# Optimization experiments

Hardware: AMD Instinct MI355X
Metric: run time of the kernel (lower is better)

Reference implementation:

```python
import jax, jax.numpy as jnp
import numpy as np
from jax import lax

B, Q, N, C = 64, 900, 100, 256
EPS = 1e-6
BOX_W, GIOU_W, CLS_W = 5.0, 2.0, 1.0


def cxcywh_to_xyxy(b):
    cx, cy, w, h = jnp.split(b, 4, axis=-1)
    return jnp.concatenate([cx - 0.5 * w, cy - 0.5 * h, cx + 0.5 * w, cy + 0.5 * h], axis=-1)


def xyxy_to_cxcywh(b):
    x0, y0, x1, y1 = jnp.split(b, 4, axis=-1)
    return jnp.concatenate([(x0 + x1) / 2, (y0 + y1) / 2, x1 - x0, y1 - y0], axis=-1)


def pairwise_giou(b1, b2):
    # b1: [Q,4] xyxy, b2: [N,4] xyxy -> [Q,N]
    area1 = (b1[:, 2] - b1[:, 0]) * (b1[:, 3] - b1[:, 1])
    area2 = (b2[:, 2] - b2[:, 0]) * (b2[:, 3] - b2[:, 1])
    lt = jnp.maximum(b1[:, None, :2], b2[None, :, :2])
    rb = jnp.minimum(b1[:, None, 2:], b2[None, :, 2:])
    wh = jnp.clip(rb - lt, 0.0)
    inter = wh[..., 0] * wh[..., 1]
    union = area1[:, None] + area2[None, :] - inter
    iou = inter / (union + EPS)
    lt2 = jnp.minimum(b1[:, None, :2], b2[None, :, :2])
    rb2 = jnp.maximum(b1[:, None, 2:], b2[None, :, 2:])
    wh2 = jnp.clip(rb2 - lt2, 0.0)
    area = wh2[..., 0] * wh2[..., 1]
    return iou - (area - union) / (area + EPS)


def elementwise_giou(b1, b2):
    # b1, b2: [..., 4] xyxy -> [...]; equals diag of pairwise giou
    area1 = (b1[..., 2] - b1[..., 0]) * (b1[..., 3] - b1[..., 1])
    area2 = (b2[..., 2] - b2[..., 0]) * (b2[..., 3] - b2[..., 1])
    lt = jnp.maximum(b1[..., :2], b2[..., :2])
    rb = jnp.minimum(b1[..., 2:], b2[..., 2:])
    wh = jnp.clip(rb - lt, 0.0)
    inter = wh[..., 0] * wh[..., 1]
    union = area1 + area2 - inter
    iou = inter / (union + EPS)
    lt2 = jnp.minimum(b1[..., :2], b2[..., :2])
    rb2 = jnp.maximum(b1[..., 2:], b2[..., 2:])
    wh2 = jnp.clip(rb2 - lt2, 0.0)
    area = wh2[..., 0] * wh2[..., 1]
    return iou - (area - union) / (area + EPS)


def greedy_match(iou_img):
    # iou_img: [Q, N]; sequentially assign best unused pred to each target (in target order)
    def step(used, col):
        idx = jnp.argmax(jnp.where(used, -jnp.inf, col))
        return used.at[idx].set(True), idx
    used0 = jnp.zeros(iou_img.shape[0], dtype=bool)
    _, idxs = lax.scan(step, used0, iou_img.T)
    return idxs  # [N]


def setup_inputs() -> dict:
    key = jax.random.key(0)
    k1, k2, k3, k4, k5 = jax.random.split(key, 5)
    pb = jax.random.uniform(k1, (B, Q, 4), dtype=jnp.float32)
    # cxcywh with small positive w,h
    pred_boxes = jnp.concatenate([pb[..., :2], pb[..., 2:] * 0.3 + 0.01], axis=-1)
    pred_logits = jax.random.normal(k2, (B, Q, C), dtype=jnp.float32)
    lo = jax.random.uniform(k3, (B, N, 2), dtype=jnp.float32) * 0.8
    sz = jax.random.uniform(k4, (B, N, 2), dtype=jnp.float32) * 0.2 + 0.01
    target_boxes = jnp.concatenate([lo, lo + sz], axis=-1)  # valid xyxy in [0,1]
    target_labels = jax.random.randint(k5, (B, N), 0, C)
    return {"pred_boxes": pred_boxes, "pred_logits": pred_logits,
            "target_boxes": target_boxes, "target_labels": target_labels}


def reference(pred_boxes, pred_logits, target_boxes, target_labels):
    pred_xyxy = cxcywh_to_xyxy(pred_boxes)                      # [B,Q,4]
    iou = lax.stop_gradient(jax.vmap(pairwise_giou)(pred_xyxy, target_boxes))  # [B,Q,N]
    idxs = jax.vmap(greedy_match)(iou)                          # [B,N] matched pred indices

    mpb = jnp.take_along_axis(pred_boxes, idxs[..., None], axis=1)   # [B,N,4] cxcywh
    mtb = xyxy_to_cxcywh(target_boxes)                               # [B,N,4]
    l1_loss = jnp.abs(mpb - mtb).sum()

    giou = elementwise_giou(cxcywh_to_xyxy(mpb), target_boxes)       # [B,N]
    giou_loss = (1.0 - giou).sum()

    ml = jnp.take_along_axis(pred_logits, idxs[..., None], axis=1)   # [B,N,C]
    tdist = jax.nn.one_hot(target_labels, ml.shape[-1], dtype=ml.dtype)
    # stable BCE-with-logits, reduction='sum'
    cls_loss = (jnp.maximum(ml, 0.0) - ml * tdist + jnp.log1p(jnp.exp(-jnp.abs(ml)))).sum()

    num_boxes = idxs.shape[0] * idxs.shape[1]
    return (BOX_W * l1_loss + GIOU_W * giou_loss + CLS_W * cls_loss) / num_boxes
```

## Files before the change

kernel.cpp:

```cpp
#include <hip/hip_runtime.h>
#include <math.h>

constexpr int B_ = 64, Q_ = 900, N_ = 100, C_ = 256;
constexpr float EPSF = 1e-6f;
constexpr float BOX_W = 5.0f, GIOU_W = 2.0f, CLS_W = 1.0f;
constexpr int KP = 15;
constexpr int K_ = 8;
typedef unsigned long long u64;
typedef unsigned int u32;

__device__ __forceinline__ float giou_f(float px0, float py0, float px1, float py1, float pa,
                                        float tx0, float ty0, float tx1, float ty1, float ta) {
    float ltx = fmaxf(px0, tx0), lty = fmaxf(py0, ty0);
    float rbx = fminf(px1, tx1), rby = fminf(py1, ty1);
    float w = fmaxf(rbx - ltx, 0.0f), h = fmaxf(rby - lty, 0.0f);
    float inter = w * h;
    float uni = pa + ta - inter;
    float iou = inter / (uni + EPSF);
    float ex0 = fminf(px0, tx0), ey0 = fminf(py0, ty0);
    float ex1 = fmaxf(px1, tx1), ey1 = fmaxf(py1, ty1);
    float ew = fmaxf(ex1 - ex0, 0.0f), eh = fmaxf(ey1 - ey0, 0.0f);
    float earea = ew * eh;
    return iou - (earea - uni) / (earea + EPSF);
}

__device__ __forceinline__ u32 f2ord(float f) {
    u32 u = __float_as_uint(f);
    return (u & 0x80000000u) ? ~u : (u | 0x80000000u);
}
__device__ __forceinline__ u64 mkkey(float g, int q) {
    return ((u64)f2ord(g) << 32) | (u32)(~(u32)q);
}
__device__ __forceinline__ int keyidx(u64 k) { return (int)(~(u32)k); }
__device__ __forceinline__ u64 umax64(u64 a, u64 b) { return a > b ? a : b; }
__device__ __forceinline__ u64 umin64(u64 a, u64 b) { return a > b ? b : a; }

__global__ __launch_bounds__(256) void cand_kernel(
    const float* __restrict__ pred_boxes,
    const float* __restrict__ target_boxes,
    u32* __restrict__ cands)
{
    const int blk = blockIdx.x;
    const int b = blk / 25;
    const int wave = threadIdx.x >> 6;
    const int lane = threadIdx.x & 63;
    const int n = (blk % 25) * 4 + wave;
    const int bn = b * N_ + n;

    const float* t = target_boxes + (size_t)bn * 4;
    float tx0 = t[0], ty0 = t[1], tx1 = t[2], ty1 = t[3];
    float ta = (tx1 - tx0) * (ty1 - ty0);

    const float4* pbv = (const float4*)(pred_boxes + (size_t)b * Q_ * 4);
    u64 a0 = 0, a1 = 0, a2 = 0, a3 = 0, a4 = 0, a5 = 0, a6 = 0, a7 = 0;
    #pragma unroll
    for (int k = 0; k < KP; ++k) {
        int q = lane + (k << 6);
        if (q < Q_) {
            float4 c = pbv[q];
            float x0 = c.x - 0.5f * c.z, y0 = c.y - 0.5f * c.w;
            float x1 = c.x + 0.5f * c.z, y1 = c.y + 0.5f * c.w;
            float pa = (x1 - x0) * (y1 - y0);
            float g = giou_f(x0, y0, x1, y1, pa, tx0, ty0, tx1, ty1, ta);
            u64 kk = mkkey(g, q);
            a7 = umax64(a7, umin64(a6, kk));
            a6 = umax64(a6, umin64(a5, kk));
            a5 = umax64(a5, umin64(a4, kk));
            a4 = umax64(a4, umin64(a3, kk));
            a3 = umax64(a3, umin64(a2, kk));
            a2 = umax64(a2, umin64(a1, kk));
            a1 = umax64(a1, umin64(a0, kk));
            a0 = umax64(a0, kk);
        }
    }
    u32* outp = cands + (size_t)bn * K_;
    #pragma unroll
    for (int j = 0; j < K_; ++j) {
        u64 m = a0;
        #pragma unroll
        for (int off = 32; off >= 1; off >>= 1) {
            u64 o = __shfl_xor(m, off);
            if (o > m) m = o;
        }
        if (lane == 0) outp[j] = (u32)keyidx(m);
        if (a0 == m) {
            a0 = a1; a1 = a2; a2 = a3; a3 = a4; a4 = a5; a5 = a6; a6 = a7; a7 = 0;
        }
    }
}

__global__ __launch_bounds__(64, 1) void match_kernel(
    const float* __restrict__ pred_boxes,
    const float* __restrict__ target_boxes,
    const u32*   __restrict__ cands,
    int* __restrict__ matches,
    double* __restrict__ box_part)
{
    const int b = blockIdx.x;
    const int lane = threadIdx.x;

    __shared__ float tx0s[N_], ty0s[N_], tx1s[N_], ty1s[N_], tas[N_];
    __shared__ int   s_ms[N_];
    __shared__ u32   s_used[32];
    __shared__ u32   s_claim[1024];

    for (int i = lane; i < 1024; i += 64) s_claim[i] = 0u;
    if (lane < 32) s_used[lane] = 0u;
    for (int n = lane; n < N_; n += 64) {
        const float* t = target_boxes + (size_t)(b * N_ + n) * 4;
        float x0 = t[0], y0 = t[1], x1 = t[2], y1 = t[3];
        tx0s[n] = x0; ty0s[n] = y0; tx1s[n] = x1; ty1s[n] = y1;
        tas[n] = (x1 - x0) * (y1 - y0);
    }

    int cA[K_], cB[K_];
    {
        const u32* p = cands + (size_t)(b * N_ + lane) * K_;
        #pragma unroll
        for (int j = 0; j < K_; ++j) cA[j] = (int)p[j];
    }
    #pragma unroll
    for (int j = 0; j < K_; ++j) cB[j] = 0;
    if (lane + 64 < N_) {
        const u32* p = cands + (size_t)(b * N_ + lane + 64) * K_;
        #pragma unroll
        for (int j = 0; j < K_; ++j) cB[j] = (int)p[j];
    }

    const float4* pbv = (const float4*)(pred_boxes + (size_t)b * Q_ * 4);
    bool activeA = true;
    bool activeB = (lane + 64 < N_);
    __syncthreads();

    int round = 1;
    while (__ballot(activeA) | __ballot(activeB)) {
        int pickA = -1, pickB = -1;
        #pragma unroll
        for (int j = 0; j < K_; ++j) {
            int ia = cA[j];
            bool availA = !((s_used[ia >> 5] >> (ia & 31)) & 1u);
            if (pickA < 0 && availA) pickA = ia;
            int ib = cB[j];
            bool availB = !((s_used[ib >> 5] >> (ib & 31)) & 1u);
            if (pickB < 0 && availB) pickB = ib;
        }
        u64 fm = __ballot(activeA && pickA < 0);
        while (fm) {
            int c = (int)__builtin_ctzll(fm);
            float tx0 = tx0s[c], ty0 = ty0s[c], tx1 = tx1s[c], ty1 = ty1s[c], ta = tas[c];
            u64 bk = 0ull;
            #pragma unroll
            for (int k = 0; k < KP; ++k) {
                int q = lane + (k << 6);
                if (q < Q_ && !((s_used[q >> 5] >> (q & 31)) & 1u)) {
                    float4 cc = pbv[q];
                    float x0 = cc.x - 0.5f * cc.z, y0 = cc.y - 0.5f * cc.w;
                    float x1 = cc.x + 0.5f * cc.z, y1 = cc.y + 0.5f * cc.w;
                    float pa = (x1 - x0) * (y1 - y0);
                    float g = giou_f(x0, y0, x1, y1, pa, tx0, ty0, tx1, ty1, ta);
                    u64 kk = mkkey(g, q);
                    if (kk > bk) bk = kk;
                }
            }
            #pragma unroll
            for (int off = 32; off >= 1; off >>= 1) {
                u64 o = __shfl_xor(bk, off);
                if (o > bk) bk = o;
            }
            if (lane == c) pickA = keyidx(bk);
            fm &= fm - 1;
        }
        fm = __ballot(activeB && pickB < 0);
        while (fm) {
            int c = (int)__builtin_ctzll(fm);
            int n = c + 64;
            float tx0 = tx0s[n], ty0 = ty0s[n], tx1 = tx1s[n], ty1 = ty1s[n], ta = tas[n];
            u64 bk = 0ull;
            #pragma unroll
            for (int k = 0; k < KP; ++k) {
                int q = lane + (k << 6);
                if (q < Q_ && !((s_used[q >> 5] >> (q & 31)) & 1u)) {
                    float4 cc = pbv[q];
                    float x0 = cc.x - 0.5f * cc.z, y0 = cc.y - 0.5f * cc.w;
                    float x1 = cc.x + 0.5f * cc.z, y1 = cc.y + 0.5f * cc.w;
                    float pa = (x1 - x0) * (y1 - y0);
                    float g = giou_f(x0, y0, x1, y1, pa, tx0, ty0, tx1, ty1, ta);
                    u64 kk = mkkey(g, q);
                    if (kk > bk) bk = kk;
                }
            }
            #pragma unroll
            for (int off = 32; off >= 1; off >>= 1) {
                u64 o = __shfl_xor(bk, off);
                if (o > bk) bk = o;
            }
            if (lane == c) pickB = keyidx(bk);
            fm &= fm - 1;
        }
        u32 tagA = ((u32)round << 16) | (0xFFFFu - (u32)lane);
        u32 tagB = ((u32)round << 16) | (0xFFFFu - (u32)(lane + 64));
        if (activeA) atomicMax(&s_claim[pickA], tagA);
        if (activeB) atomicMax(&s_claim[pickB], tagB);
        __syncthreads();
        if (activeA && s_claim[pickA] == tagA) {
            s_ms[lane] = pickA;
            atomicOr(&s_used[pickA >> 5], 1u << (pickA & 31));
            activeA = false;
        }
        if (activeB && s_claim[pickB] == tagB) {
            s_ms[lane + 64] = pickB;
            atomicOr(&s_used[pickB >> 5], 1u << (pickB & 31));
            activeB = false;
        }
        __syncthreads();
        ++round;
    }

    double acc = 0.0;
    for (int n = lane; n < N_; n += 64) {
        int q = s_ms[n];
        matches[b * N_ + n] = q;
        float4 c = pbv[q];
        float tx0 = tx0s[n], ty0 = ty0s[n], tx1 = tx1s[n], ty1 = ty1s[n];
        float tcx = (tx0 + tx1) * 0.5f, tcy = (ty0 + ty1) * 0.5f;
        float tw = tx1 - tx0, th = ty1 - ty0;
        float l1 = fabsf(c.x - tcx) + fabsf(c.y - tcy) + fabsf(c.z - tw) + fabsf(c.w - th);
        float x0 = c.x - 0.5f * c.z, y0 = c.y - 0.5f * c.w;
        float x1 = c.x + 0.5f * c.z, y1 = c.y + 0.5f * c.w;
        float pa2 = (x1 - x0) * (y1 - y0);
        float g = giou_f(x0, y0, x1, y1, pa2, tx0, ty0, tx1, ty1, tas[n]);
        acc += (double)(BOX_W * l1) + (double)(GIOU_W * (1.0f - g));
    }
    #pragma unroll
    for (int off = 32; off >= 1; off >>= 1) acc += __shfl_xor(acc, off);
    if (lane == 0) box_part[b] = acc;
}

__global__ __launch_bounds__(64) void bce_kernel(
    const float* __restrict__ pred_logits,
    const int* __restrict__ target_labels,
    const int* __restrict__ matches,
    double* __restrict__ part)
{
    const int bn = blockIdx.x;
    const int b = bn / N_;
    const int lane = threadIdx.x;
    const int q = matches[bn];
    const int lab = target_labels[bn];

    const float4* row = (const float4*)(pred_logits + ((size_t)(b * Q_ + q)) * C_);
    float4 v = row[lane];
    int base = lane * 4;
    float xs[4] = {v.x, v.y, v.z, v.w};
    double acc = 0.0;
    #pragma unroll
    for (int j = 0; j < 4; ++j) {
        float x = xs[j];
        float t = (base + j == lab) ? 1.0f : 0.0f;
        float term = fmaxf(x, 0.0f) - x * t + log1pf(expf(-fabsf(x)));
        acc += (double)term;
    }
    #pragma unroll
    for (int off = 32; off >= 1; off >>= 1) acc += __shfl_xor(acc, off);
    if (lane == 0) part[bn] = acc * (double)CLS_W;
}

__global__ __launch_bounds__(256) void finalize_kernel(
    const double* __restrict__ bce_part,
    const double* __restrict__ box_part,
    float* __restrict__ out)
{
    const int tid = threadIdx.x;
    double acc = 0.0;
    for (int i = tid; i < B_ * N_; i += 256) acc += bce_part[i];
    if (tid < B_) acc += box_part[tid];
    __shared__ double red[256];
    red[tid] = acc;
    __syncthreads();
    #pragma unroll
    for (int s = 128; s >= 1; s >>= 1) {
        if (tid < s) red[tid] += red[tid + s];
        __syncthreads();
    }
    if (tid == 0) out[0] = (float)(red[0] / (double)(B_ * N_));
}

extern "C" void kernel_launch(void* const* d_in, const int* in_sizes, int n_in,
                              void* d_out, int out_size, void* d_ws, size_t ws_size,
                              hipStream_t stream) {
    const float* pred_boxes    = (const float*)d_in[0];
    const float* pred_logits   = (const float*)d_in[1];
    const float* target_boxes  = (const float*)d_in[2];
    const int*   target_labels = (const int*)d_in[3];
    float* out = (float*)d_out;

    char* ws = (char*)d_ws;
    u32*    cands    = (u32*)(ws);
    int*    matches  = (int*)(ws + 204800);
    double* bce_part = (double*)(ws + 230400);
    double* box_part = (double*)(ws + 281600);

    hipLaunchKernelGGL(cand_kernel, dim3(1600), dim3(256), 0, stream,
                       pred_boxes, target_boxes, cands);
    hipLaunchKernelGGL(match_kernel, dim3(B_), dim3(64), 0, stream,
                       pred_boxes, target_boxes, cands, matches, box_part);
    hipLaunchKernelGGL(bce_kernel, dim3(B_ * N_), dim3(64), 0, stream,
                       pred_logits, target_labels, matches, bce_part);
    hipLaunchKernelGGL(finalize_kernel, dim3(1), dim3(256), 0, stream,
                       bce_part, box_part, out);
}
```

Baseline: 46.01 us.

## Fuse matching, BCE and final reduction into one kernel with last-block finalize

```diff
diff --git a/kernel.cpp b/kernel.cpp
--- a/kernel.cpp
+++ b/kernel.cpp
@@ -32,14 +32,15 @@
     return ((u64)f2ord(g) << 32) | (u32)(~(u32)q);
 }
 __device__ __forceinline__ int keyidx(u64 k) { return (int)(~(u32)k); }
-__device__ __forceinline__ u64 umax64(u64 a, u64 b) { return a > b ? a : b; }
-__device__ __forceinline__ u64 umin64(u64 a, u64 b) { return a > b ? b : a; }
 
 __global__ __launch_bounds__(256) void cand_kernel(
     const float* __restrict__ pred_boxes,
     const float* __restrict__ target_boxes,
-    u32* __restrict__ cands)
+    u32* __restrict__ cands,
+    u32* __restrict__ cnt)
 {
+    if (blockIdx.x == 0 && threadIdx.x == 0) *cnt = 0u;
+
     const int blk = blockIdx.x;
     const int b = blk / 25;
     const int wave = threadIdx.x >> 6;
@@ -52,65 +53,81 @@
     float ta = (tx1 - tx0) * (ty1 - ty0);
 
     const float4* pbv = (const float4*)(pred_boxes + (size_t)b * Q_ * 4);
-    u64 a0 = 0, a1 = 0, a2 = 0, a3 = 0, a4 = 0, a5 = 0, a6 = 0, a7 = 0;
+
+    u32 ordv[KP];
     #pragma unroll
     for (int k = 0; k < KP; ++k) {
         int q = lane + (k << 6);
+        ordv[k] = 0u;
         if (q < Q_) {
             float4 c = pbv[q];
             float x0 = c.x - 0.5f * c.z, y0 = c.y - 0.5f * c.w;
             float x1 = c.x + 0.5f * c.z, y1 = c.y + 0.5f * c.w;
             float pa = (x1 - x0) * (y1 - y0);
             float g = giou_f(x0, y0, x1, y1, pa, tx0, ty0, tx1, ty1, ta);
-            u64 kk = mkkey(g, q);
-            a7 = umax64(a7, umin64(a6, kk));
-            a6 = umax64(a6, umin64(a5, kk));
-            a5 = umax64(a5, umin64(a4, kk));
-            a4 = umax64(a4, umin64(a3, kk));
-            a3 = umax64(a3, umin64(a2, kk));
-            a2 = umax64(a2, umin64(a1, kk));
-            a1 = umax64(a1, umin64(a0, kk));
-            a0 = umax64(a0, kk);
-        }
-    }
-    u32* outp = cands + (size_t)bn * K_;
+            ordv[k] = f2ord(g);
+        }
+    }
+
+    u32 alive = 0x7FFFu;
+    u32 o8[K_];
     #pragma unroll
     for (int j = 0; j < K_; ++j) {
-        u64 m = a0;
+        u32 bo = 0u; int bk = 0;
+        #pragma unroll
+        for (int k = 0; k < KP; ++k) {
+            bool tk = (((alive >> k) & 1u) != 0u) && (ordv[k] > bo);
+            bo = tk ? ordv[k] : bo;
+            bk = tk ? k : bk;
+        }
+        u64 myk = ((u64)bo << 32) | (u32)(~(u32)(lane + (bk << 6)));
+        u64 m = myk;
         #pragma unroll
         for (int off = 32; off >= 1; off >>= 1) {
             u64 o = __shfl_xor(m, off);
             if (o > m) m = o;
         }
-        if (lane == 0) outp[j] = (u32)keyidx(m);
-        if (a0 == m) {
-            a0 = a1; a1 = a2; a2 = a3; a3 = a4; a4 = a5; a5 = a6; a6 = a7; a7 = 0;
-        }
-    }
-}
-
-__global__ __launch_bounds__(64, 1) void match_kernel(
+        if (myk == m) alive &= ~(1u << bk);
+        o8[j] = (u32)(~(u32)m);
+    }
+    if (lane == 0) {
+        uint4* outp = (uint4*)(cands + (size_t)bn * K_);
+        outp[0] = make_uint4(o8[0], o8[1], o8[2], o8[3]);
+        outp[1] = make_uint4(o8[4], o8[5], o8[6], o8[7]);
+    }
+}
+
+__global__ __launch_bounds__(256) void fused_kernel(
     const float* __restrict__ pred_boxes,
+    const float* __restrict__ pred_logits,
     const float* __restrict__ target_boxes,
+    const int*   __restrict__ target_labels,
     const u32*   __restrict__ cands,
-    int* __restrict__ matches,
-    double* __restrict__ box_part)
+    double* __restrict__ partial,
+    u32* __restrict__ cnt,
+    float* __restrict__ out)
 {
     const int b = blockIdx.x;
-    const int lane = threadIdx.x;
+    const int tid = threadIdx.x;
+    const int lane = tid & 63;
 
     __shared__ float tx0s[N_], ty0s[N_], tx1s[N_], ty1s[N_], tas[N_];
     __shared__ int   s_ms[N_];
+    __shared__ int   labs[N_];
     __shared__ u32   s_used[32];
     __shared__ u32   s_claim[1024];
-
-    for (int i = lane; i < 1024; i += 64) s_claim[i] = 0u;
-    if (lane < 32) s_used[lane] = 0u;
-    for (int n = lane; n < N_; n += 64) {
-        const float* t = target_boxes + (size_t)(b * N_ + n) * 4;
+    __shared__ double red[256];
+    __shared__ int   s_last;
+
+    #pragma unroll
+    for (int i = 0; i < 4; ++i) s_claim[tid + i * 256] = 0u;
+    if (tid < 32) s_used[tid] = 0u;
+    if (tid < N_) {
+        const float* t = target_boxes + (size_t)(b * N_ + tid) * 4;
         float x0 = t[0], y0 = t[1], x1 = t[2], y1 = t[3];
-        tx0s[n] = x0; ty0s[n] = y0; tx1s[n] = x1; ty1s[n] = y1;
-        tas[n] = (x1 - x0) * (y1 - y0);
+        tx0s[tid] = x0; ty0s[tid] = y0; tx1s[tid] = x1; ty1s[tid] = y1;
+        tas[tid] = (x1 - x0) * (y1 - y0);
+        labs[tid] = target_labels[b * N_ + tid];
     }
 
     int cA[K_], cB[K_];
@@ -217,64 +234,36 @@
     }
 
     double acc = 0.0;
-    for (int n = lane; n < N_; n += 64) {
-        int q = s_ms[n];
-        matches[b * N_ + n] = q;
+
+    if (tid < N_) {
+        int q = s_ms[tid];
         float4 c = pbv[q];
-        float tx0 = tx0s[n], ty0 = ty0s[n], tx1 = tx1s[n], ty1 = ty1s[n];
+        float tx0 = tx0s[tid], ty0 = ty0s[tid], tx1 = tx1s[tid], ty1 = ty1s[tid];
         float tcx = (tx0 + tx1) * 0.5f, tcy = (ty0 + ty1) * 0.5f;
         float tw = tx1 - tx0, th = ty1 - ty0;
         float l1 = fabsf(c.x - tcx) + fabsf(c.y - tcy) + fabsf(c.z - tw) + fabsf(c.w - th);
         float x0 = c.x - 0.5f * c.z, y0 = c.y - 0.5f * c.w;
         float x1 = c.x + 0.5f * c.z, y1 = c.y + 0.5f * c.w;
-        float pa2 = (x1 - x0) * (y1 - y0);
-        float g = giou_f(x0, y0, x1, y1, pa2, tx0, ty0, tx1, ty1, tas[n]);
+        float pa = (x1 - x0) * (y1 - y0);
+        float g = giou_f(x0, y0, x1, y1, pa, tx0, ty0, tx1, ty1, tas[tid]);
         acc += (double)(BOX_W * l1) + (double)(GIOU_W * (1.0f - g));
     }
-    #pragma unroll
-    for (int off = 32; off >= 1; off >>= 1) acc += __shfl_xor(acc, off);
-    if (lane == 0) box_part[b] = acc;
-}
-
-__global__ __launch_bounds__(64) void bce_kernel(
-    const float* __restrict__ pred_logits,
-    const int* __restrict__ target_labels,
-    const int* __restrict__ matches,
-    double* __restrict__ part)
-{
-    const int bn = blockIdx.x;
-    const int b = bn / N_;
-    const int lane = threadIdx.x;
-    const int q = matches[bn];
-    const int lab = target_labels[bn];
-
-    const float4* row = (const float4*)(pred_logits + ((size_t)(b * Q_ + q)) * C_);
-    float4 v = row[lane];
-    int base = lane * 4;
-    float xs[4] = {v.x, v.y, v.z, v.w};
-    double acc = 0.0;
-    #pragma unroll
-    for (int j = 0; j < 4; ++j) {
-        float x = xs[j];
-        float t = (base + j == lab) ? 1.0f : 0.0f;
-        float term = fmaxf(x, 0.0f) - x * t + log1pf(expf(-fabsf(x)));
-        acc += (double)term;
-    }
-    #pragma unroll
-    for (int off = 32; off >= 1; off >>= 1) acc += __shfl_xor(acc, off);
-    if (lane == 0) part[bn] = acc * (double)CLS_W;
-}
-
-__global__ __launch_bounds__(256) void finalize_kernel(
-    const double* __restrict__ bce_part,
-    const double* __restrict__ box_part,
-    float* __restrict__ out)
-{
-    const int tid = threadIdx.x;
-    double acc = 0.0;
-    for (int i = tid; i < B_ * N_; i += 256) acc += bce_part[i];
-    if (tid < B_) acc += box_part[tid];
-    __shared__ double red[256];
+
+    {
+        const float* lg = pred_logits + (size_t)b * Q_ * C_ + tid;
+        double e0 = 0.0, e1 = 0.0;
+        #pragma unroll 4
+        for (int n = 0; n < N_; ++n) {
+            int q = s_ms[n];
+            int lab = labs[n];
+            float x = lg[(size_t)q * C_];
+            float tt = (tid == lab) ? 1.0f : 0.0f;
+            float term = fmaxf(x, 0.0f) - x * tt + log1pf(expf(-fabsf(x)));
+            if (n & 1) e1 += (double)term; else e0 += (double)term;
+        }
+        acc += (double)CLS_W * (e0 + e1);
+    }
+
     red[tid] = acc;
     __syncthreads();
     #pragma unroll
@@ -282,7 +271,19 @@
         if (tid < s) red[tid] += red[tid + s];
         __syncthreads();
     }
-    if (tid == 0) out[0] = (float)(red[0] / (double)(B_ * N_));
+
+    if (tid == 0) {
+        __hip_atomic_store(&partial[b], red[0], __ATOMIC_RELEASE, __HIP_MEMORY_SCOPE_AGENT);
+        u32 old = __hip_atomic_fetch_add(cnt, 1u, __ATOMIC_ACQ_REL, __HIP_MEMORY_SCOPE_AGENT);
+        s_last = (old == (u32)(B_ - 1)) ? 1 : 0;
+    }
+    __syncthreads();
+    if (s_last && tid < 64) {
+        double v = __hip_atomic_load(&partial[lane], __ATOMIC_ACQUIRE, __HIP_MEMORY_SCOPE_AGENT);
+        #pragma unroll
+        for (int off = 32; off >= 1; off >>= 1) v += __shfl_xor(v, off);
+        if (lane == 0) out[0] = (float)(v / (double)(B_ * N_));
+    }
 }
 
 extern "C" void kernel_launch(void* const* d_in, const int* in_sizes, int n_in,
@@ -295,17 +296,13 @@
     float* out = (float*)d_out;
 
     char* ws = (char*)d_ws;
-    u32*    cands    = (u32*)(ws);
-    int*    matches  = (int*)(ws + 204800);
-    double* bce_part = (double*)(ws + 230400);
-    double* box_part = (double*)(ws + 281600);
+    u32*    cands   = (u32*)(ws);
+    double* partial = (double*)(ws + 204800);
+    u32*    cnt     = (u32*)(ws + 205312);
 
     hipLaunchKernelGGL(cand_kernel, dim3(1600), dim3(256), 0, stream,
-                       pred_boxes, target_boxes, cands);
-    hipLaunchKernelGGL(match_kernel, dim3(B_), dim3(64), 0, stream,
-                       pred_boxes, target_boxes, cands, matches, box_part);
-    hipLaunchKernelGGL(bce_kernel, dim3(B_ * N_), dim3(64), 0, stream,
-                       pred_logits, target_labels, matches, bce_part);
-    hipLaunchKernelGGL(finalize_kernel, dim3(1), dim3(256), 0, stream,
-                       bce_part, box_part, out);
-}
+                       pred_boxes, target_boxes, cands, cnt);
+    hipLaunchKernelGGL(fused_kernel, dim3(B_), dim3(256), 0, stream,
+                       pred_boxes, pred_logits, target_boxes, target_labels,
+                       cands, partial, cnt, out);
+}
```

Measured after the change: 60.64 us. 1.32x slower.
